# Kernel optimization log

Measured on AMD Instinct MI355X. Metric: run time of the kernel, lower is better.

## Reference

```python
import jax, jax.numpy as jnp
import numpy as np

# DH-SFNN: 2 dendritic LIF layers (denri, no tanh, reset-by-subtraction) + leaky readout integrator.
GAMMA = 0.5   # surrogate gradient scale
LENS = 0.5    # surrogate gradient width
VTH = 1.0     # spike threshold
DT = 1.0

@jax.custom_vjp
def spike_fn(x):
    # Heaviside forward, Gaussian surrogate backward (act_fun_adp)
    return (x > 0.0).astype(x.dtype)

def _spike_fwd(x):
    return spike_fn(x), x

def _spike_bwd(x, g):
    sg = GAMMA * jnp.exp(-x * x / (2.0 * LENS * LENS)) / (jnp.sqrt(2.0 * jnp.pi) * LENS)
    return (g * sg,)

spike_fn.defvjp(_spike_fwd, _spike_bwd)

B, T, IN, H, O, K = 256, 250, 700, 256, 20, 4  # batch, time, in_dim, hidden, out_dim, branch
WARMUP = 10


def _branch_mask(rng, out_dim, in_dim, k):
    # Each neuron's k branches see a disjoint random partition of the inputs.
    m = np.zeros((out_dim * k, in_dim), np.float32)
    step = in_dim // k
    for i in range(out_dim):
        perm = rng.permutation(in_dim)
        for j in range(k):
            m[i * k + j, perm[j * step:(j + 1) * step]] = 1.0
    return m


def setup_inputs() -> dict:
    key = jax.random.key(0)
    ks = jax.random.split(key, 12)
    rng = np.random.default_rng(0)
    s1 = 1.0 / np.sqrt(IN)
    s2 = 1.0 / np.sqrt(H)
    # branch-masked dense weights (apply_mask() already baked in)
    W1 = jax.random.uniform(ks[0], (H * K, IN), minval=-s1, maxval=s1) * jnp.asarray(_branch_mask(rng, H, IN, K))
    b1 = jax.random.uniform(ks[1], (H * K,), minval=-s1, maxval=s1)
    tau_n1 = jax.random.uniform(ks[2], (H, K), minval=2.0, maxval=6.0)
    tau_m1 = jax.random.uniform(ks[3], (H,), minval=0.0, maxval=4.0)
    W2 = jax.random.uniform(ks[4], (H * K, H), minval=-s2, maxval=s2) * jnp.asarray(_branch_mask(rng, H, H, K))
    b2 = jax.random.uniform(ks[5], (H * K,), minval=-s2, maxval=s2)
    tau_n2 = jax.random.uniform(ks[6], (H, K), minval=2.0, maxval=6.0)
    tau_m2 = jax.random.uniform(ks[7], (H,), minval=0.0, maxval=4.0)
    Wr = jax.random.uniform(ks[8], (O, H), minval=-s2, maxval=s2)
    br = jax.random.uniform(ks[9], (O,), minval=-s2, maxval=s2)
    tau_mr = jax.random.uniform(ks[10], (O,), minval=0.0, maxval=4.0)
    # sparse binary spike train input (SHD-like)
    x = (jax.random.uniform(ks[11], (B, T, IN)) < 0.1).astype(jnp.float32)
    return dict(x=x, W1=W1, b1=b1, tau_n1=tau_n1, tau_m1=tau_m1,
                W2=W2, b2=b2, tau_n2=tau_n2, tau_m2=tau_m2,
                Wr=Wr, br=br, tau_mr=tau_mr, warmup=WARMUP)


def reference(x, W1, b1, tau_n1, tau_m1, W2, b2, tau_n2, tau_m2, Wr, br, tau_mr, warmup):
    Bb, Tt, _ = x.shape
    beta1 = jax.nn.sigmoid(tau_n1)   # [H,K] dendritic decay
    alpha1 = jax.nn.sigmoid(tau_m1)  # [H]   soma decay
    beta2 = jax.nn.sigmoid(tau_n2)
    alpha2 = jax.nn.sigmoid(tau_m2)
    alphar = jax.nn.sigmoid(tau_mr)  # [O]

    def dense_branch(inp, W, b):
        return (inp @ W.T + b).reshape(inp.shape[0], -1, K)  # [B,H,K]

    def step(carry, xt):
        d1, m1, s1, d2, m2, s2, mr, acc, t = carry
        # layer 1: dendritic filtering then LIF with soft reset
        d1 = beta1 * d1 + (1.0 - beta1) * dense_branch(xt, W1, b1)
        m1 = m1 * alpha1 + (1.0 - alpha1) * DT * d1.sum(-1) - VTH * s1
        s1 = spike_fn(m1 - VTH)
        # layer 2
        d2 = beta2 * d2 + (1.0 - beta2) * dense_branch(s1, W2, b2)
        m2 = m2 * alpha2 + (1.0 - alpha2) * DT * d2.sum(-1) - VTH * s2
        s2 = spike_fn(m2 - VTH)
        # leaky readout integrator
        mr = mr * alphar + (1.0 - alphar) * (s2 @ Wr.T + br)
        acc = acc + jnp.where(t >= warmup, mr, jnp.zeros_like(mr))
        return (d1, m1, s1, d2, m2, s2, mr, acc, t + 1), None

    z = lambda *s: jnp.zeros(s, x.dtype)
    carry0 = (z(Bb, H, K), z(Bb, H), z(Bb, H),
              z(Bb, H, K), z(Bb, H), z(Bb, H),
              z(Bb, O), z(Bb, O), jnp.int32(0))
    carry, _ = jax.lax.scan(step, carry0, jnp.moveaxis(x, 1, 0))
    acc = carry[7]
    return acc / (Tt - warmup)  # readout_mode == 'mean'
```

## Files before the change

### kernel.cpp

```cpp
#include <hip/hip_runtime.h>
#include <hip/hip_bf16.h>

typedef unsigned short us16;
typedef unsigned int u32;
typedef unsigned long long ull;

#define B_   256
#define T_   250
#define IN_  700
#define KP_  704
#define H_   256
#define O_   20
#define HK_  1024
#define NPAIR_ (B_ * T_)
#define LDP_ 40
#define CP_  136

typedef __attribute__((ext_vector_type(8))) short short8;
typedef __attribute__((ext_vector_type(4))) float f32x4;

__device__ __forceinline__ float bfbits(unsigned int lo16) {
    union { unsigned int i; float f; } v; v.i = lo16 << 16; return v.f;
}
__device__ __forceinline__ float bflo(unsigned int u) {
    union { unsigned int i; float f; } v; v.i = u << 16; return v.f;
}
__device__ __forceinline__ float bfhi(unsigned int u) {
    union { unsigned int i; float f; } v; v.i = u & 0xffff0000u; return v.f;
}
__device__ __forceinline__ us16 f2bfu(float f) {
    __hip_bfloat16 h = __float2bfloat16(f);
    union { __hip_bfloat16 h; us16 u; } c; c.h = h; return c.u;
}
__device__ __forceinline__ float sigm(float x) { return 1.0f / (1.0f + expf(-x)); }
__device__ __forceinline__ int rfl(int v) { return __builtin_amdgcn_readfirstlane(v); }

__device__ __forceinline__ bool detect_bf16(const us16* __restrict__ taun) {
    int ok = 0;
#pragma unroll
    for (int i = 0; i < 8; i += 2) ok += ((taun[i] >> 8) == 0x40) ? 1 : 0;
    return ok == 4;
}
__device__ __forceinline__ float ldany(const void* __restrict__ p, long i, bool isb) {
    return isb ? bfbits(((const us16*)p)[i]) : ((const float*)p)[i];
}

__device__ __forceinline__ void async_cp16(const us16* g, us16* l) {
    __builtin_amdgcn_global_load_lds(
        (const __attribute__((address_space(1))) u32*)g,
        (__attribute__((address_space(3))) u32*)l, 16, 0, 0);
}

#define BAR_LDS() do {                                                   \
    asm volatile("s_waitcnt lgkmcnt(0)\n\ts_barrier" ::: "memory");      \
} while (0)

__global__ __launch_bounds__(256) void cvt_rows2(
    const void* __restrict__ xin, const void* __restrict__ w1in,
    us16* __restrict__ xout, us16* __restrict__ w1out,
    const us16* __restrict__ taun) {
    const bool isb = detect_bf16(taun);
    const int r = blockIdx.x * 4 + (threadIdx.x >> 6);
    const int l = threadIdx.x & 63;
    const void* in; us16* out; long ibase, obase;
    if (r < NPAIR_) {
        in = xin;  out = xout;  ibase = (long)r * IN_; obase = (long)r * KP_;
    } else {
        const int r2 = r - NPAIR_;
        if (r2 >= HK_) return;
        in = w1in; out = w1out; ibase = (long)r2 * IN_; obase = (long)r2 * KP_;
    }
    for (int c = l; c < 88; c += 64) {
        uint4 o;
        if (c < 87) {
            if (isb) {
                uint2 lo = *(const uint2*)((const us16*)in + ibase + 8 * c);
                uint2 hi = *(const uint2*)((const us16*)in + ibase + 8 * c + 4);
                o.x = lo.x; o.y = lo.y; o.z = hi.x; o.w = hi.y;
            } else {
                float4 f0 = *(const float4*)((const float*)in + ibase + 8 * c);
                float4 f1 = *(const float4*)((const float*)in + ibase + 8 * c + 4);
                o.x = (u32)f2bfu(f0.x) | ((u32)f2bfu(f0.y) << 16);
                o.y = (u32)f2bfu(f0.z) | ((u32)f2bfu(f0.w) << 16);
                o.z = (u32)f2bfu(f1.x) | ((u32)f2bfu(f1.y) << 16);
                o.w = (u32)f2bfu(f1.z) | ((u32)f2bfu(f1.w) << 16);
            }
        } else {
            o.z = 0u; o.w = 0u;
            if (isb) {
                uint2 lo = *(const uint2*)((const us16*)in + ibase + 696);
                o.x = lo.x; o.y = lo.y;
            } else {
                float4 f0 = *(const float4*)((const float*)in + ibase + 696);
                o.x = (u32)f2bfu(f0.x) | ((u32)f2bfu(f0.y) << 16);
                o.y = (u32)f2bfu(f0.z) | ((u32)f2bfu(f0.w) << 16);
            }
        }
        *(uint4*)(out + obase + 8 * c) = o;
    }
}

__global__ void transpose_to_bf16(const void* __restrict__ in, us16* __restrict__ out,
                                  int R, int C, const us16* __restrict__ taun) {
    const bool isb = detect_bf16(taun);
    __shared__ us16 tile[32][33];
    int c0 = blockIdx.x * 32, r0 = blockIdx.y * 32;
    int tx = threadIdx.x, ty = threadIdx.y;
#pragma unroll
// ... 65 lines not shown
    __syncthreads();

    for (int s = 0; s < 11; ++s) {
        const int cur = (s & 1) * 16384;
        const int nxt = 16384 - cur;
        if (s + 1 < 11) {
            const int kb = (s + 1) * 64;
#pragma unroll
            for (int i = 0; i < 4; ++i) async_cp16(xg[i] + kb, smem + nxt + asl[i]);
#pragma unroll
            for (int i = 0; i < 4; ++i) async_cp16(wg[i] + kb, smem + nxt + bsl[i]);
        }

        short8 af[4][2], bfv[4][2];
#pragma unroll
        for (int i = 0; i < 4; ++i) {
            af[i][0]  = *(const short8*)(smem + cur + aoff0[i]);
            af[i][1]  = *(const short8*)(smem + cur + aoff1[i]);
            bfv[i][0] = *(const short8*)(smem + cur + boff0[i]);
            bfv[i][1] = *(const short8*)(smem + cur + boff1[i]);
        }
#pragma unroll
        for (int h = 0; h < 2; ++h)
#pragma unroll
            for (int i = 0; i < 4; ++i)
#pragma unroll
                for (int j = 0; j < 4; ++j)
                    acc[i][j] = __builtin_amdgcn_mfma_f32_16x16x32_bf16(
                        af[i][h], bfv[j][h], acc[i][j], 0, 0, 0);

        __syncthreads();
    }

#pragma unroll
    for (int i = 0; i < 4; ++i)
#pragma unroll
        for (int j = 0; j < 4; ++j)
#pragma unroll
            for (int r = 0; r < 4; ++r)
                smem[(wr * 64 + i * 16 + quad * 4 + r) * CP_ +
                     (wc * 64 + j * 16 + l16)] = f2bfu(acc[i][j][r]);
    __syncthreads();
    {
        const int c8 = (lane & 15) * 8;
#pragma unroll
        for (int r2 = 0; r2 < 8; ++r2) {
            const int row = w * 32 + r2 * 4 + (lane >> 4);
            const uint4 v = *(const uint4*)(smem + row * CP_ + c8);
            *(uint4*)(Apre + (long)(m0 + row) * HK_ + n0 + c8) = v;
        }
    }
}

__global__ __launch_bounds__(256) void dhsfnn_4w(
    const us16* __restrict__ Apre,
    const void* __restrict__ b1,  const void* __restrict__ tau_n1,
    const void* __restrict__ tau_m1,
    const void* __restrict__ b2,  const void* __restrict__ tau_n2,
    const void* __restrict__ tau_m2,
    const void* __restrict__ Wr,  const void* __restrict__ br,
    const void* __restrict__ tau_mr,
    const us16* __restrict__ W2T,
    const int* __restrict__ warmup_p,
    void* __restrict__ out)
{
    __shared__ ull msk1[2][4];
    __shared__ ull msk2[2][4];

    const int tid  = threadIdx.x;
    const int lane = tid & 63;
    const int w    = tid >> 6;
    const int b    = blockIdx.x;
    const bool isb = detect_bf16((const us16*)tau_n1);
    const int wu   = *warmup_p;

    float be1[4], cb1[4], ce1[4], be2[4], cb2[4], ce2[4], d1[4], d2[4];
#pragma unroll
    for (int k = 0; k < 4; ++k) {
        const long gi = 4L * tid + k;
        const float t1 = sigm(ldany(tau_n1, gi, isb));
        be1[k] = t1; ce1[k] = 1.f - t1; cb1[k] = ce1[k] * ldany(b1, gi, isb);
        const float t2 = sigm(ldany(tau_n2, gi, isb));
        be2[k] = t2; ce2[k] = 1.f - t2; cb2[k] = ce2[k] * ldany(b2, gi, isb);
        d1[k] = 0.f; d2[k] = 0.f;
    }
    const float al1 = sigm(ldany(tau_m1, tid, isb)), cal1 = 1.f - al1;
    const float al2 = sigm(ldany(tau_m2, tid, isb)), cal2 = 1.f - al2;
    float m1 = 0.f, s1f = 0.f, m2 = 0.f, s2f = 0.f;
    float alr = 0.f, brv = 0.f;
    if (tid < O_) { alr = sigm(ldany(tau_mr, tid, isb)); brv = ldany(br, tid, isb); }
    float mrv = 0.f, accO = 0.f;

    const us16* ap = Apre + (long)b * T_ * HK_ + 4 * tid;

    uint2 q0 = *(const uint2*)(ap);
    uint2 q1 = *(const uint2*)(ap + HK_);
    uint2 q2 = *(const uint2*)(ap + 2 * HK_);
    uint2 q3 = *(const uint2*)(ap + 3 * HK_);

    {
        const float a0 = bflo(q0.x), a1 = bfhi(q0.x), a2 = bflo(q0.y), a3 = bfhi(q0.y);
        d1[0] = be1[0] * d1[0] + cb1[0] + ce1[0] * a0;
        d1[1] = be1[1] * d1[1] + cb1[1] + ce1[1] * a1;
        d1[2] = be1[2] * d1[2] + cb1[2] + ce1[2] * a2;
        d1[3] = be1[3] * d1[3] + cb1[3] + ce1[3] * a3;
        const float s = (d1[0] + d1[1]) + (d1[2] + d1[3]);
        m1 = m1 * al1 + cal1 * s - s1f;
        s1f = (m1 > 1.0f) ? 1.f : 0.f;
        const ull bm = __ballot(s1f > 0.f);
        if (lane == 0) msk1[0][w] = bm;
    }
    BAR_LDS();

    auto body = [&](int t, uint2& q, bool doL1) {
        const ull p0 = msk1[t & 1][0], p1 = msk1[t & 1][1];
        const ull p2 = msk1[t & 1][2], p3 = msk1[t & 1][3];
        d2[0] = be2[0] * d2[0] + cb2[0];
        d2[1] = be2[1] * d2[1] + cb2[1];
        d2[2] = be2[2] * d2[2] + cb2[2];
        d2[3] = be2[3] * d2[3] + cb2[3];
        if ((p0 | p1 | p2 | p3) != 0ull) {
            float g0 = 0.f, g1 = 0.f, g2 = 0.f, g3 = 0.f;
#pragma unroll
            for (int w2 = 0; w2 < 4; ++w2) {
                ull mm = (w2 == 0) ? p0 : (w2 == 1) ? p1 : (w2 == 2) ? p2 : p3;
                while (mm) {
                    const int i = __ffsll(mm) - 1; mm &= mm - 1;
                    const int n = 64 * w2 + i;
                    const uint2 wv = *(const uint2*)(W2T + ((long)n << 10) + 4 * tid);
                    g0 += bflo(wv.x); g1 += bfhi(wv.x);
                    g2 += bflo(wv.y); g3 += bfhi(wv.y);
                }
            }
            d2[0] += ce2[0] * g0; d2[1] += ce2[1] * g1;
            d2[2] += ce2[2] * g2; d2[3] += ce2[3] * g3;
        }
        const float s2s = (d2[0] + d2[1]) + (d2[2] + d2[3]);
        m2 = m2 * al2 + cal2 * s2s - s2f;
        s2f = (m2 > 1.0f) ? 1.f : 0.f;
        const ull b2m = __ballot(s2f > 0.f);
        if (lane == 0) msk2[t & 1][w] = b2m;

        if (doL1) {
            const float a0 = bflo(q.x), a1 = bfhi(q.x), a2 = bflo(q.y), a3 = bfhi(q.y);
            if (t + 5 < T_) q = *(const uint2*)(ap + (long)(t + 5) * HK_);
            d1[0] = be1[0] * d1[0] + cb1[0] + ce1[0] * a0;
            d1[1] = be1[1] * d1[1] + cb1[1] + ce1[1] * a1;
            d1[2] = be1[2] * d1[2] + cb1[2] + ce1[2] * a2;
            d1[3] = be1[3] * d1[3] + cb1[3] + ce1[3] * a3;
            const float s = (d1[0] + d1[1]) + (d1[2] + d1[3]);
            m1 = m1 * al1 + cal1 * s - s1f;
            s1f = (m1 > 1.0f) ? 1.f : 0.f;
            const ull b1m = __ballot(s1f > 0.f);
            if (lane == 0) msk1[(t + 1) & 1][w] = b1m;
        }

        BAR_LDS();

        if (w == 0) {
            const ull r0 = msk2[t & 1][0], r1 = msk2[t & 1][1];
            const ull r2 = msk2[t & 1][2], r3 = msk2[t & 1][3];
            if (lane < O_) {
                float sum = brv;
                if ((r0 | r1 | r2 | r3) != 0ull) {
#pragma unroll
                    for (int w2 = 0; w2 < 4; ++w2) {
                        ull mm = (w2 == 0) ? r0 : (w2 == 1) ? r1 : (w2 == 2) ? r2 : r3;
                        while (mm) {
                            const int i = __ffsll(mm) - 1; mm &= mm - 1;
                            sum += ldany(Wr, (long)lane * H_ + 64 * w2 + i, isb);
                        }
                    }
                }
                mrv = alr * mrv + (1.f - alr) * sum;
                if (t >= wu) accO += mrv;
            }
        }
    };

    int t = 0;
    for (int it = 0; it < 62; ++it) {
        body(t + 0, q1, true);
        body(t + 1, q2, true);
        body(t + 2, q3, true);
        body(t + 3, q0, true);
        t += 4;
    }
    body(248, q1, true);
    body(249, q2, false);

    if (tid < O_) {
        const float res = accO / (float)(T_ - wu);
        if (isb) ((us16*)out)[b * O_ + tid] = f2bfu(res);
        else     ((float*)out)[b * O_ + tid] = res;
    }
}

#define GA_LOAD(S, AV, BV) do {                                               \
    const int k0_ = (S) * 32 + half16;                                        \
    if (k0_ + 16 <= IN_) {                                                    \
        if (isb) {                                                            \
            const us16* pa_ = (const us16*)X  + arow + k0_;                   \
            const us16* pb_ = (const us16*)W1 + brow + k0_;                   \
            uint2 a0_ = *(const uint2*)pa_,        a1_ = *(const uint2*)(pa_ + 4);  \
            uint2 a2_ = *(const uint2*)(pa_ + 8),  a3_ = *(const uint2*)(pa_ + 12); \
            uint2 b0_ = *(const uint2*)pb_,        b1_ = *(const uint2*)(pb_ + 4);  \
            uint2 b2_ = *(const uint2*)(pb_ + 8),  b3_ = *(const uint2*)(pb_ + 12); \
            AV[0]=a0_.x; AV[1]=a0_.y; AV[2]=a1_.x; AV[3]=a1_.y;               \
            AV[4]=a2_.x; AV[5]=a2_.y; AV[6]=a3_.x; AV[7]=a3_.y;               \
            BV[0]=b0_.x; BV[1]=b0_.y; BV[2]=b1_.x; BV[3]=b1_.y;               \
            BV[4]=b2_.x; BV[5]=b2_.y; BV[6]=b3_.x; BV[7]=b3_.y;               \
        } else {                                                              \
            const float* pa_ = (const float*)X  + arow + k0_;                 \
            const float* pb_ = (const float*)W1 + brow + k0_;                 \
            float4 fa0_ = *(const float4*)pa_,        fa1_ = *(const float4*)(pa_ + 4);  \
            float4 fa2_ = *(const float4*)(pa_ + 8),  fa3_ = *(const float4*)(pa_ + 12); \
            float4 fb0_ = *(const float4*)pb_,        fb1_ = *(const float4*)(pb_ + 4);  \
            float4 fb2_ = *(const float4*)(pb_ + 8),  fb3_ = *(const float4*)(pb_ + 12); \
            AV[0] = (unsigned)f2bfu(fa0_.x) | ((unsigned)f2bfu(fa0_.y) << 16); \
            AV[1] = (unsigned)f2bfu(fa0_.z) | ((unsigned)f2bfu(fa0_.w) << 16); \
            AV[2] = (unsigned)f2bfu(fa1_.x) | ((unsigned)f2bfu(fa1_.y) << 16); \
            AV[3] = (unsigned)f2bfu(fa1_.z) | ((unsigned)f2bfu(fa1_.w) << 16); \
            AV[4] = (unsigned)f2bfu(fa2_.x) | ((unsigned)f2bfu(fa2_.y) << 16); \
            AV[5] = (unsigned)f2bfu(fa2_.z) | ((unsigned)f2bfu(fa2_.w) << 16); \
            AV[6] = (unsigned)f2bfu(fa3_.x) | ((unsigned)f2bfu(fa3_.y) << 16); \
            AV[7] = (unsigned)f2bfu(fa3_.z) | ((unsigned)f2bfu(fa3_.w) << 16); \
            BV[0] = (unsigned)f2bfu(fb0_.x) | ((unsigned)f2bfu(fb0_.y) << 16); \
            BV[1] = (unsigned)f2bfu(fb0_.z) | ((unsigned)f2bfu(fb0_.w) << 16); \
            BV[2] = (unsigned)f2bfu(fb1_.x) | ((unsigned)f2bfu(fb1_.y) << 16); \
            BV[3] = (unsigned)f2bfu(fb1_.z) | ((unsigned)f2bfu(fb1_.w) << 16); \
            BV[4] = (unsigned)f2bfu(fb2_.x) | ((unsigned)f2bfu(fb2_.y) << 16); \
            BV[5] = (unsigned)f2bfu(fb2_.z) | ((unsigned)f2bfu(fb2_.w) << 16); \
            BV[6] = (unsigned)f2bfu(fb3_.x) | ((unsigned)f2bfu(fb3_.y) << 16); \
            BV[7] = (unsigned)f2bfu(fb3_.z) | ((unsigned)f2bfu(fb3_.w) << 16); \
        }                                                                     \
    } else {                                                                  \
        _Pragma("unroll")                                                     \
        for (int e_ = 0; e_ < 8; ++e_) { AV[e_] = 0u; BV[e_] = 0u; }          \
        _Pragma("unroll")                                                     \
        for (int e_ = 0; e_ < 16; ++e_) {                                     \
            int k_ = k0_ + e_;                                                \
            if (k_ < IN_) {                                                   \
                unsigned va_ = (unsigned)f2bfu(ldany(X,  arow + k_, isb));    \
                unsigned vb_ = (unsigned)f2bfu(ldany(W1, brow + k_, isb));    \
                AV[e_ >> 1] |= va_ << ((e_ & 1) * 16);                        \
                BV[e_ >> 1] |= vb_ << ((e_ & 1) * 16);                        \
            }                                                                 \
// ... 60 lines not shown
    }

    const long arow = (long)(m0 + ra) * IN_;
    const long brow = (long)(n0 + ra) * IN_;
    us16* asw = As + ra * LDP_ + half16;
    us16* bsw = Bs + ra * LDP_ + half16;

    unsigned av0[8], bv0[8], av1[8], bv1[8];
    GA_LOAD(0, av0, bv0);

    for (int ss = 0; ss < 11; ++ss) {
        __syncthreads();
        GA_STORE(av0, bv0);
        __syncthreads();
        GA_LOAD(2 * ss + 1, av1, bv1);
        GA_MFMA();
        __syncthreads();
        GA_STORE(av1, bv1);
        __syncthreads();
        if (ss < 10) GA_LOAD(2 * ss + 2, av0, bv0);
        GA_MFMA();
    }

#pragma unroll
    for (int i = 0; i < 4; ++i) {
#pragma unroll
        for (int j = 0; j < 4; ++j) {
            const int gm = m0 + wr * 64 + i * 16 + quad * 4;
            const int gn = n0 + wc * 64 + j * 16 + l16;
            us16* op = Apre + (long)gm * HK_ + gn;
#pragma unroll
            for (int r = 0; r < 4; ++r)
                op[(long)r * HK_] = f2bfu(acc[i][j][r]);
        }
    }
}

__global__ __launch_bounds__(64) void dhsfnn_wave(
    const us16* __restrict__ Apre,
    const void* __restrict__ b1,  const void* __restrict__ tau_n1,
    const void* __restrict__ tau_m1,
    const void* __restrict__ b2,  const void* __restrict__ tau_n2,
    const void* __restrict__ tau_m2,
    const void* __restrict__ Wr,  const void* __restrict__ br,
    const void* __restrict__ tau_mr,
    const us16* __restrict__ W2T,
    const int* __restrict__ warmup_p,
    void* __restrict__ out)
{
    const int lane = threadIdx.x;
    const int b    = blockIdx.x;
    const bool isb = detect_bf16((const us16*)tau_n1);
    const int wu   = *warmup_p;

    float be1[16], cb1[16], be2[16], cb2[16], d1[16], d2[16];
#pragma unroll
    for (int e = 0; e < 16; ++e) {
        const long gi = (long)lane * 16 + e;
        const float t1 = sigm(ldany(tau_n1, gi, isb));
        be1[e] = t1; cb1[e] = (1.f - t1) * ldany(b1, gi, isb);
        const float t2 = sigm(ldany(tau_n2, gi, isb));
        be2[e] = t2; cb2[e] = (1.f - t2) * ldany(b2, gi, isb);
        d1[e] = 0.f; d2[e] = 0.f;
    }
    float al1[4], al2[4], m1[4], s1[4], m2[4], s2[4];
#pragma unroll
    for (int j = 0; j < 4; ++j) {
        al1[j] = sigm(ldany(tau_m1, lane * 4 + j, isb));
        al2[j] = sigm(ldany(tau_m2, lane * 4 + j, isb));
        m1[j] = 0.f; s1[j] = 0.f; m2[j] = 0.f; s2[j] = 0.f;
    }
    float alr = 0.f, brv = 0.f;
    if (lane < O_) { alr = sigm(ldany(tau_mr, lane, isb)); brv = ldany(br, lane, isb); }
    float mrv = 0.f, accO = 0.f;

    const us16* ap = Apre + (long)b * T_ * HK_ + lane * 16;

    auto wstep = [&](int t, uint4 lo, uint4 hi) {
        float a[16];
        a[0]=bflo(lo.x);  a[1]=bfhi(lo.x);  a[2]=bflo(lo.y);  a[3]=bfhi(lo.y);
        a[4]=bflo(lo.z);  a[5]=bfhi(lo.z);  a[6]=bflo(lo.w);  a[7]=bfhi(lo.w);
        a[8]=bflo(hi.x);  a[9]=bfhi(hi.x);  a[10]=bflo(hi.y); a[11]=bfhi(hi.y);
        a[12]=bflo(hi.z); a[13]=bfhi(hi.z); a[14]=bflo(hi.w); a[15]=bfhi(hi.w);
#pragma unroll
        for (int e = 0; e < 16; ++e)
            d1[e] = be1[e] * d1[e] + cb1[e] + (1.f - be1[e]) * a[e];
        unsigned long long bal1[4];
#pragma unroll
        for (int j = 0; j < 4; ++j) {
            const float s = (d1[j*4+0] + d1[j*4+1]) + (d1[j*4+2] + d1[j*4+3]);
            m1[j] = m1[j] * al1[j] + (1.f - al1[j]) * s - s1[j];
            s1[j] = (m1[j] > 1.0f) ? 1.f : 0.f;
            bal1[j] = __ballot(s1[j] > 0.f);
        }
        if ((bal1[0] | bal1[1] | bal1[2] | bal1[3]) != 0ull) {
            float g[16];
#pragma unroll
            for (int e = 0; e < 16; ++e) g[e] = 0.f;
            for (int j2 = 0; j2 < 4; ++j2) {
                unsigned long long mm = bal1[j2];
                while (mm) {
                    const int i = __ffsll(mm) - 1; mm &= mm - 1;
                    const us16* wv = W2T + ((long)(i * 4 + j2) << 10) + lane * 16;
                    const uint4 wl = *(const uint4*)wv;
                    const uint4 wh = *(const uint4*)(wv + 8);
                    g[0]+=bflo(wl.x);  g[1]+=bfhi(wl.x);  g[2]+=bflo(wl.y);  g[3]+=bfhi(wl.y);
                    g[4]+=bflo(wl.z);  g[5]+=bfhi(wl.z);  g[6]+=bflo(wl.w);  g[7]+=bfhi(wl.w);
                    g[8]+=bflo(wh.x);  g[9]+=bfhi(wh.x);  g[10]+=bflo(wh.y); g[11]+=bfhi(wh.y);
                    g[12]+=bflo(wh.z); g[13]+=bfhi(wh.z); g[14]+=bflo(wh.w); g[15]+=bfhi(wh.w);
                }
            }
#pragma unroll
            for (int e = 0; e < 16; ++e)
                d2[e] = be2[e] * d2[e] + cb2[e] + (1.f - be2[e]) * g[e];
        } else {
#pragma unroll
            for (int e = 0; e < 16; ++e)
                d2[e] = be2[e] * d2[e] + cb2[e];
        }
        unsigned long long bal2[4];
#pragma unroll
        for (int j = 0; j < 4; ++j) {
            const float s = (d2[j*4+0] + d2[j*4+1]) + (d2[j*4+2] + d2[j*4+3]);
            m2[j] = m2[j] * al2[j] + (1.f - al2[j]) * s - s2[j];
            s2[j] = (m2[j] > 1.0f) ? 1.f : 0.f;
            bal2[j] = __ballot(s2[j] > 0.f);
        }
        if (lane < O_) {
            float sum = brv;
            if ((bal2[0] | bal2[1] | bal2[2] | bal2[3]) != 0ull) {
                for (int j2 = 0; j2 < 4; ++j2) {
                    unsigned long long mm = bal2[j2];
                    while (mm) {
                        const int i = __ffsll(mm) - 1; mm &= mm - 1;
                        sum += ldany(Wr, (long)lane * H_ + (i * 4 + j2), isb);
                    }
                }
            }
            mrv = alr * mrv + (1.f - alr) * sum;
            if (t >= wu) accO += mrv;
        }
    };

    uint4 q0a = *(const uint4*)(ap);
    uint4 q0b = *(const uint4*)(ap + 8);
    uint4 q1a = *(const uint4*)(ap + HK_);
    uint4 q1b = *(const uint4*)(ap + HK_ + 8);
    uint4 q2a = *(const uint4*)(ap + 2 * HK_);
    uint4 q2b = *(const uint4*)(ap + 2 * HK_ + 8);
    uint4 q3a = *(const uint4*)(ap + 3 * HK_);
    uint4 q3b = *(const uint4*)(ap + 3 * HK_ + 8);

    int t = 0;
    for (int it = 0; it < 62; ++it) {
        wstep(t + 0, q0a, q0b);
        q0a = *(const uint4*)(ap + (long)(t + 4) * HK_);
        q0b = *(const uint4*)(ap + (long)(t + 4) * HK_ + 8);
        wstep(t + 1, q1a, q1b);
        if (t + 5 < T_) {
            q1a = *(const uint4*)(ap + (long)(t + 5) * HK_);
            q1b = *(const uint4*)(ap + (long)(t + 5) * HK_ + 8);
        }
        wstep(t + 2, q2a, q2b);
        if (t + 6 < T_) {
            q2a = *(const uint4*)(ap + (long)(t + 6) * HK_);
            q2b = *(const uint4*)(ap + (long)(t + 6) * HK_ + 8);
        }
        wstep(t + 3, q3a, q3b);
        if (t + 7 < T_) {
            q3a = *(const uint4*)(ap + (long)(t + 7) * HK_);
            q3b = *(const uint4*)(ap + (long)(t + 7) * HK_ + 8);
        }
        t += 4;
    }
    wstep(248, q0a, q0b);
    wstep(249, q1a, q1b);

    if (lane < O_) {
        const float res = accO / (float)(T_ - wu);
        if (isb) ((us16*)out)[b * O_ + lane] = f2bfu(res);
        else     ((float*)out)[b * O_ + lane] = res;
    }
}

__global__ __launch_bounds__(256) void dhsfnn_fb(
    const void* __restrict__ x,  const void* __restrict__ W1,
    const void* __restrict__ b1, const void* __restrict__ tau_n1,
    const void* __restrict__ tau_m1,
    const void* __restrict__ W2, const void* __restrict__ b2,
    const void* __restrict__ tau_n2, const void* __restrict__ tau_m2,
    const void* __restrict__ Wr, const void* __restrict__ br,
    const void* __restrict__ tau_mr,
    const int* __restrict__ warmup_p,
    void* __restrict__ out)
{
    __shared__ us16 list1[1024];
    __shared__ us16 list2[256];
    __shared__ us16 list3[256];
    __shared__ int n1s, n2s, n3s;

    const int tid = threadIdx.x;
    const int b   = blockIdx.x;
    const int h   = tid;
    const bool isb = detect_bf16((const us16*)tau_n1);
    const int wu  = *warmup_p;

    const float be1_0 = sigm(ldany(tau_n1, 4 * h + 0, isb));
    const float be1_1 = sigm(ldany(tau_n1, 4 * h + 1, isb));
    const float be1_2 = sigm(ldany(tau_n1, 4 * h + 2, isb));
    const float be1_3 = sigm(ldany(tau_n1, 4 * h + 3, isb));
    const float bi1_0 = ldany(b1, 4 * h + 0, isb), bi1_1 = ldany(b1, 4 * h + 1, isb);
    const float bi1_2 = ldany(b1, 4 * h + 2, isb), bi1_3 = ldany(b1, 4 * h + 3, isb);
    const float al1 = sigm(ldany(tau_m1, h, isb));
    const float be2_0 = sigm(ldany(tau_n2, 4 * h + 0, isb));
    const float be2_1 = sigm(ldany(tau_n2, 4 * h + 1, isb));
    const float be2_2 = sigm(ldany(tau_n2, 4 * h + 2, isb));
    const float be2_3 = sigm(ldany(tau_n2, 4 * h + 3, isb));
    const float bi2_0 = ldany(b2, 4 * h + 0, isb), bi2_1 = ldany(b2, 4 * h + 1, isb);
    const float bi2_2 = ldany(b2, 4 * h + 2, isb), bi2_3 = ldany(b2, 4 * h + 3, isb);
    const float al2 = sigm(ldany(tau_m2, h, isb));
    float alr = 0.f, brv = 0.f;
    if (h < O_) { alr = sigm(ldany(tau_mr, h, isb)); brv = ldany(br, h, isb); }

    float d1_0 = 0.f, d1_1 = 0.f, d1_2 = 0.f, d1_3 = 0.f, m1v = 0.f, s1f = 0.f;
    float d2_0 = 0.f, d2_1 = 0.f, d2_2 = 0.f, d2_3 = 0.f, m2v = 0.f, s2f = 0.f;
    float mrv = 0.f, accO = 0.f;

    const long xbase = (long)b * T_ * IN_;
    float xv0 = ldany(x, xbase + tid, isb);
    float xv1 = ldany(x, xbase + tid + 256, isb);
    float xv2 = (tid + 512 < IN_) ? ldany(x, xbase + tid + 512, isb) : 0.f;

    for (int t = 0; t < T_; ++t) {
        const bool p0 = xv0 != 0.f, p1 = xv1 != 0.f, p2 = xv2 != 0.f;
        if (t + 1 < T_) {
// ... 55 lines not shown
        __syncthreads();
        int n3 = n3s; n3 = (n3 < 256) ? n3 : 256;

        if (h < O_) {
            float sum = brv;
            for (int idx = 0; idx < n3; ++idx) {
                int j = (int)list3[idx];
                j = (j < H_) ? j : (H_ - 1);
                sum += ldany(Wr, (long)h * H_ + j, isb);
            }
            mrv = alr * mrv + (1.f - alr) * sum;
            if (t >= wu) accO += mrv;
        }
    }
    if (h < O_) {
        float res = accO / (float)(T_ - wu);
        if (isb) ((us16*)out)[b * O_ + h] = f2bfu(res);
        else     ((float*)out)[b * O_ + h] = res;
    }
}

extern "C" void kernel_launch(void* const* d_in, const int* in_sizes, int n_in,
                              void* d_out, int out_size, void* d_ws, size_t ws_size,
                              hipStream_t stream) {
    const void* x      = d_in[0];
    const void* W1     = d_in[1];
    const void* b1     = d_in[2];
    const void* tau_n1 = d_in[3];
    const void* tau_m1 = d_in[4];
    const void* W2     = d_in[5];
    const void* b2     = d_in[6];
    const void* tau_n2 = d_in[7];
    const void* tau_m2 = d_in[8];
    const void* Wr     = d_in[9];
    const void* br     = d_in[10];
    const void* tau_mr = d_in[11];
    const int*  warmup = (const int*)d_in[12];

    const size_t w2t_bytes  = (size_t)H_ * HK_ * 2;
    const size_t xbf_bytes  = (size_t)NPAIR_ * KP_ * 2;
    const size_t w1b_bytes  = (size_t)HK_ * KP_ * 2;
    const size_t apre_bytes = (size_t)NPAIR_ * HK_ * 2;

    const bool tier0 = (d_ws != nullptr &&
                        ws_size >= w2t_bytes + xbf_bytes + w1b_bytes + apre_bytes);
    const bool tier1 = (d_ws != nullptr && ws_size >= w2t_bytes + apre_bytes);

    dim3 blk(32, 8);
    if (tier0) {
        us16* W2T  = (us16*)d_ws;
        us16* Xbf  = (us16*)((char*)d_ws + w2t_bytes);
        us16* W1bf = (us16*)((char*)d_ws + w2t_bytes + xbf_bytes);
        us16* Apre = (us16*)((char*)d_ws + w2t_bytes + xbf_bytes + w1b_bytes);
        cvt_rows2<<<(NPAIR_ + HK_) / 4, 256, 0, stream>>>(
            x, W1, Xbf, W1bf, (const us16*)tau_n1);
        transpose_to_bf16<<<dim3((H_ + 31) / 32, (HK_ + 31) / 32), blk, 0, stream>>>(
            W2, W2T, HK_, H_, (const us16*)tau_n1);
        gemm_bf<<<4096, 256, 0, stream>>>(Xbf, W1bf, Apre);
        dhsfnn_4w<<<B_, 256, 0, stream>>>(
            Apre, b1, tau_n1, tau_m1, b2, tau_n2, tau_m2,
            Wr, br, tau_mr, W2T, warmup, d_out);
    } else if (tier1) {
        us16* W2T  = (us16*)d_ws;
        us16* Apre = (us16*)((char*)d_ws + w2t_bytes);
        transpose_to_bf16<<<dim3((H_ + 31) / 32, (HK_ + 31) / 32), blk, 0, stream>>>(
            W2, W2T, HK_, H_, (const us16*)tau_n1);
        gemm_apre<<<4096, 256, 0, stream>>>(x, W1, (const us16*)tau_n1, Apre);
        dhsfnn_wave<<<B_, 64, 0, stream>>>(
            Apre, b1, tau_n1, tau_m1, b2, tau_n2, tau_m2,
            Wr, br, tau_mr, W2T, warmup, d_out);
    } else {
        dhsfnn_fb<<<B_, 256, 0, stream>>>(x, W1, b1, tau_n1, tau_m1,
                                          W2, b2, tau_n2, tau_m2,
                                          Wr, br, tau_mr, warmup, d_out);
    }
}
```

Measured before the change: 456.1 us.

## Split recurrence into layer-1 spike check and conditional full recurrence

Measured after the change: 409.6 us. -10.2%, faster.

```diff
diff --git a/kernel.cpp b/kernel.cpp
--- a/kernel.cpp
+++ b/kernel.cpp
@@ -50,10 +50,6 @@
         (const __attribute__((address_space(1))) u32*)g,
         (__attribute__((address_space(3))) u32*)l, 16, 0, 0);
 }
-
-#define BAR_LDS() do {                                                   \
-    asm volatile("s_waitcnt lgkmcnt(0)\n\ts_barrier" ::: "memory");      \
-} while (0)
 
 __global__ __launch_bounds__(256) void cvt_rows2(
     const void* __restrict__ xin, const void* __restrict__ w1in,
@@ -225,7 +221,272 @@
     }
 }
 
-__global__ __launch_bounds__(256) void dhsfnn_4w(
+__device__ void wave_recur(
+    const us16* __restrict__ Apre,
+    const void* __restrict__ b1,  const void* __restrict__ tau_n1,
+    const void* __restrict__ tau_m1,
+    const void* __restrict__ b2,  const void* __restrict__ tau_n2,
+    const void* __restrict__ tau_m2,
+    const void* __restrict__ Wr,  const void* __restrict__ br,
+    const void* __restrict__ tau_mr,
+    const us16* __restrict__ W2T,
+    int wu, bool isb, int b, int lane,
+    void* __restrict__ out)
+{
+    float be1[16], cb1[16], be2[16], cb2[16], d1[16], d2[16];
+#pragma unroll
+    for (int e = 0; e < 16; ++e) {
+        const long gi = (long)lane * 16 + e;
+        const float t1 = sigm(ldany(tau_n1, gi, isb));
+        be1[e] = t1; cb1[e] = (1.f - t1) * ldany(b1, gi, isb);
+        const float t2 = sigm(ldany(tau_n2, gi, isb));
+        be2[e] = t2; cb2[e] = (1.f - t2) * ldany(b2, gi, isb);
+        d1[e] = 0.f; d2[e] = 0.f;
+    }
+    float al1[4], al2[4], m1[4], s1[4], m2[4], s2[4];
+#pragma unroll
+    for (int j = 0; j < 4; ++j) {
+        al1[j] = sigm(ldany(tau_m1, lane * 4 + j, isb));
+        al2[j] = sigm(ldany(tau_m2, lane * 4 + j, isb));
+        m1[j] = 0.f; s1[j] = 0.f; m2[j] = 0.f; s2[j] = 0.f;
+    }
+    float alr = 0.f, brv = 0.f;
+    if (lane < O_) { alr = sigm(ldany(tau_mr, lane, isb)); brv = ldany(br, lane, isb); }
+    float mrv = 0.f, accO = 0.f;
+
+    const us16* ap = Apre + (long)b * T_ * HK_ + lane * 16;
+
+    auto wstep = [&](int t, uint4 lo, uint4 hi) {
+        float a[16];
+        a[0]=bflo(lo.x);  a[1]=bfhi(lo.x);  a[2]=bflo(lo.y);  a[3]=bfhi(lo.y);
+        a[4]=bflo(lo.z);  a[5]=bfhi(lo.z);  a[6]=bflo(lo.w);  a[7]=bfhi(lo.w);
+        a[8]=bflo(hi.x);  a[9]=bfhi(hi.x);  a[10]=bflo(hi.y); a[11]=bfhi(hi.y);
+        a[12]=bflo(hi.z); a[13]=bfhi(hi.z); a[14]=bflo(hi.w); a[15]=bfhi(hi.w);
+#pragma unroll
+        for (int e = 0; e < 16; ++e)
+            d1[e] = be1[e] * d1[e] + cb1[e] + (1.f - be1[e]) * a[e];
+        unsigned long long bal1[4];
+#pragma unroll
+        for (int j = 0; j < 4; ++j) {
+            const float s = (d1[j*4+0] + d1[j*4+1]) + (d1[j*4+2] + d1[j*4+3]);
+            m1[j] = m1[j] * al1[j] + (1.f - al1[j]) * s - s1[j];
+            s1[j] = (m1[j] > 1.0f) ? 1.f : 0.f;
+            bal1[j] = __ballot(s1[j] > 0.f);
+        }
+        if ((bal1[0] | bal1[1] | bal1[2] | bal1[3]) != 0ull) {
+            float g[16];
+#pragma unroll
+            for (int e = 0; e < 16; ++e) g[e] = 0.f;
+            for (int j2 = 0; j2 < 4; ++j2) {
+                unsigned long long mm = bal1[j2];
+                while (mm) {
+                    const int i = __ffsll(mm) - 1; mm &= mm - 1;
+                    const us16* wv = W2T + ((long)(i * 4 + j2) << 10) + lane * 16;
+                    const uint4 wl = *(const uint4*)wv;
+                    const uint4 wh = *(const uint4*)(wv + 8);
+                    g[0]+=bflo(wl.x);  g[1]+=bfhi(wl.x);  g[2]+=bflo(wl.y);  g[3]+=bfhi(wl.y);
+                    g[4]+=bflo(wl.z);  g[5]+=bfhi(wl.z);  g[6]+=bflo(wl.w);  g[7]+=bfhi(wl.w);
+                    g[8]+=bflo(wh.x);  g[9]+=bfhi(wh.x);  g[10]+=bflo(wh.y); g[11]+=bfhi(wh.y);
+                    g[12]+=bflo(wh.z); g[13]+=bfhi(wh.z); g[14]+=bflo(wh.w); g[15]+=bfhi(wh.w);
+                }
+            }
+#pragma unroll
+            for (int e = 0; e < 16; ++e)
+                d2[e] = be2[e] * d2[e] + cb2[e] + (1.f - be2[e]) * g[e];
+        } else {
+#pragma unroll
+            for (int e = 0; e < 16; ++e)
+                d2[e] = be2[e] * d2[e] + cb2[e];
+        }
+        unsigned long long bal2[4];
+#pragma unroll
+        for (int j = 0; j < 4; ++j) {
+            const float s = (d2[j*4+0] + d2[j*4+1]) + (d2[j*4+2] + d2[j*4+3]);
+            m2[j] = m2[j] * al2[j] + (1.f - al2[j]) * s - s2[j];
+            s2[j] = (m2[j] > 1.0f) ? 1.f : 0.f;
+            bal2[j] = __ballot(s2[j] > 0.f);
+        }
+        if (lane < O_) {
+            float sum = brv;
+            if ((bal2[0] | bal2[1] | bal2[2] | bal2[3]) != 0ull) {
+                for (int j2 = 0; j2 < 4; ++j2) {
+                    unsigned long long mm = bal2[j2];
+                    while (mm) {
+                        const int i = __ffsll(mm) - 1; mm &= mm - 1;
+                        sum += ldany(Wr, (long)lane * H_ + (i * 4 + j2), isb);
+                    }
+                }
+            }
+            mrv = alr * mrv + (1.f - alr) * sum;
+            if (t >= wu) accO += mrv;
+        }
+    };
+
+    uint4 q0a = *(const uint4*)(ap);
+    uint4 q0b = *(const uint4*)(ap + 8);
+    uint4 q1a = *(const uint4*)(ap + HK_);
+    uint4 q1b = *(const uint4*)(ap + HK_ + 8);
+    uint4 q2a = *(const uint4*)(ap + 2 * HK_);
+    uint4 q2b = *(const uint4*)(ap + 2 * HK_ + 8);
+    uint4 q3a = *(const uint4*)(ap + 3 * HK_);
+    uint4 q3b = *(const uint4*)(ap + 3 * HK_ + 8);
+
+    int t = 0;
+    for (int it = 0; it < 62; ++it) {
+        wstep(t + 0, q0a, q0b);
+        q0a = *(const uint4*)(ap + (long)(t + 4) * HK_);
+        q0b = *(const uint4*)(ap + (long)(t + 4) * HK_ + 8);
+        wstep(t + 1, q1a, q1b);
+        if (t + 5 < T_) {
+            q1a = *(const uint4*)(ap + (long)(t + 5) * HK_);
+            q1b = *(const uint4*)(ap + (long)(t + 5) * HK_ + 8);
+        }
+        wstep(t + 2, q2a, q2b);
+        if (t + 6 < T_) {
+            q2a = *(const uint4*)(ap + (long)(t + 6) * HK_);
+            q2b = *(const uint4*)(ap + (long)(t + 6) * HK_ + 8);
+        }
+        wstep(t + 3, q3a, q3b);
+        if (t + 7 < T_) {
+            q3a = *(const uint4*)(ap + (long)(t + 7) * HK_);
+            q3b = *(const uint4*)(ap + (long)(t + 7) * HK_ + 8);
+        }
+        t += 4;
+    }
+    wstep(248, q0a, q0b);
+    wstep(249, q1a, q1b);
+
+    if (lane < O_) {
+        const float res = accO / (float)(T_ - wu);
+        if (isb) ((us16*)out)[b * O_ + lane] = f2bfu(res);
+        else     ((float*)out)[b * O_ + lane] = res;
+    }
+}
+
+__global__ __launch_bounds__(256) void l1_check(
+    const us16* __restrict__ Apre,
+    const void* __restrict__ b1,  const void* __restrict__ tau_n1,
+    const void* __restrict__ tau_m1,
+    const void* __restrict__ b2,  const void* __restrict__ tau_n2,
+    const void* __restrict__ tau_m2,
+    const void* __restrict__ Wr,  const void* __restrict__ br,
+    const void* __restrict__ tau_mr,
+    const int* __restrict__ warmup_p,
+    int* __restrict__ flags, float* __restrict__ sh_out)
+{
+    const int tid = threadIdx.x;
+    const int b   = blockIdx.x;
+    const bool isb = detect_bf16((const us16*)tau_n1);
+
+    if (b == B_) {
+        if (tid >= 64) return;
+        const int lane = tid;
+        const int wu   = *warmup_p;
+        float be2[16], cb2[16], d2[16];
+#pragma unroll
+        for (int e = 0; e < 16; ++e) {
+            const long gi = (long)lane * 16 + e;
+            const float t2 = sigm(ldany(tau_n2, gi, isb));
+            be2[e] = t2; cb2[e] = (1.f - t2) * ldany(b2, gi, isb);
+            d2[e] = 0.f;
+        }
+        float al2[4], m2[4], s2[4];
+#pragma unroll
+        for (int j = 0; j < 4; ++j) {
+            al2[j] = sigm(ldany(tau_m2, lane * 4 + j, isb));
+            m2[j] = 0.f; s2[j] = 0.f;
+        }
+        float alr = 0.f, brv = 0.f;
+        if (lane < O_) { alr = sigm(ldany(tau_mr, lane, isb)); brv = ldany(br, lane, isb); }
+        float mrv = 0.f, accO = 0.f;
+
+        for (int t = 0; t < T_; ++t) {
+#pragma unroll
+            for (int e = 0; e < 16; ++e)
+                d2[e] = be2[e] * d2[e] + cb2[e];
+            unsigned long long bal2[4];
+#pragma unroll
+            for (int j = 0; j < 4; ++j) {
+                const float s = (d2[j*4+0] + d2[j*4+1]) + (d2[j*4+2] + d2[j*4+3]);
+                m2[j] = m2[j] * al2[j] + (1.f - al2[j]) * s - s2[j];
+                s2[j] = (m2[j] > 1.0f) ? 1.f : 0.f;
+                bal2[j] = __ballot(s2[j] > 0.f);
+            }
+            if (lane < O_) {
+                float sum = brv;
+                if ((bal2[0] | bal2[1] | bal2[2] | bal2[3]) != 0ull) {
+                    for (int j2 = 0; j2 < 4; ++j2) {
+                        unsigned long long mm = bal2[j2];
+                        while (mm) {
+                            const int i = __ffsll(mm) - 1; mm &= mm - 1;
+                            sum += ldany(Wr, (long)lane * H_ + (i * 4 + j2), isb);
+                        }
+                    }
+                }
+                mrv = alr * mrv + (1.f - alr) * sum;
+                if (t >= wu) accO += mrv;
+            }
+        }
+        if (lane < O_) sh_out[lane] = accO / (float)(T_ - wu);
+        return;
+    }
+
+    __shared__ int blkflag;
+    if (tid == 0) blkflag = 0;
+    __syncthreads();
+
+    float be1[4], cb1[4], ce1[4], d1[4];
+#pragma unroll
+    for (int k = 0; k < 4; ++k) {
+        const long gi = 4L * tid + k;
+        const float t1 = sigm(ldany(tau_n1, gi, isb));
+        be1[k] = t1; ce1[k] = 1.f - t1; cb1[k] = ce1[k] * ldany(b1, gi, isb);
+        d1[k] = 0.f;
+    }
+    const float al1 = sigm(ldany(tau_m1, tid, isb)), cal1 = 1.f - al1;
+    float m1 = 0.f, s1f = 0.f;
+    int any = 0;
+
+    const us16* ap = Apre + (long)b * T_ * HK_ + 4 * tid;
+
+    uint2 q0 = *(const uint2*)(ap);
+    uint2 q1 = *(const uint2*)(ap + HK_);
+    uint2 q2 = *(const uint2*)(ap + 2 * HK_);
+    uint2 q3 = *(const uint2*)(ap + 3 * HK_);
+    uint2 q4 = *(const uint2*)(ap + 4 * HK_);
+    uint2 q5 = *(const uint2*)(ap + 5 * HK_);
+    uint2 q6 = *(const uint2*)(ap + 6 * HK_);
+    uint2 q7 = *(const uint2*)(ap + 7 * HK_);
+
+    auto body = [&](int t, uint2& q) {
+        const float a0 = bflo(q.x), a1 = bfhi(q.x), a2 = bflo(q.y), a3 = bfhi(q.y);
+        if (t + 8 < T_) q = *(const uint2*)(ap + (long)(t + 8) * HK_);
+        d1[0] = be1[0] * d1[0] + cb1[0] + ce1[0] * a0;
+        d1[1] = be1[1] * d1[1] + cb1[1] + ce1[1] * a1;
+        d1[2] = be1[2] * d1[2] + cb1[2] + ce1[2] * a2;
+        d1[3] = be1[3] * d1[3] + cb1[3] + ce1[3] * a3;
+        const float s = (d1[0] + d1[1]) + (d1[2] + d1[3]);
+        m1 = m1 * al1 + cal1 * s - s1f;
+        const int sp = (m1 > 1.0f) ? 1 : 0;
+        s1f = sp ? 1.f : 0.f;
+        any |= sp;
+    };
+
+    int t = 0;
+    for (int it = 0; it < 31; ++it) {
+        body(t + 0, q0); body(t + 1, q1); body(t + 2, q2); body(t + 3, q3);
+        body(t + 4, q4); body(t + 5, q5); body(t + 6, q6); body(t + 7, q7);
+        t += 8;
+    }
+    body(248, q0);
+    body(249, q1);
+
+    if (any) blkflag = 1;
+    __syncthreads();
+    if (tid == 0) flags[b] = blkflag;
+}
+
+__global__ __launch_bounds__(64) void finalize(
     const us16* __restrict__ Apre,
     const void* __restrict__ b1,  const void* __restrict__ tau_n1,
     const void* __restrict__ tau_m1,
@@ -235,137 +496,21 @@
     const void* __restrict__ tau_mr,
     const us16* __restrict__ W2T,
     const int* __restrict__ warmup_p,
+    const int* __restrict__ flags, const float* __restrict__ sh_out,
     void* __restrict__ out)
 {
-    __shared__ ull msk1[2][4];
-    __shared__ ull msk2[2][4];
-
-    const int tid  = threadIdx.x;
-    const int lane = tid & 63;
-    const int w    = tid >> 6;
+    const int lane = threadIdx.x;
     const int b    = blockIdx.x;
     const bool isb = detect_bf16((const us16*)tau_n1);
     const int wu   = *warmup_p;
 
-    float be1[4], cb1[4], ce1[4], be2[4], cb2[4], ce2[4], d1[4], d2[4];
-#pragma unroll
-    for (int k = 0; k < 4; ++k) {
-        const long gi = 4L * tid + k;
-        const float t1 = sigm(ldany(tau_n1, gi, isb));
-        be1[k] = t1; ce1[k] = 1.f - t1; cb1[k] = ce1[k] * ldany(b1, gi, isb);
-        const float t2 = sigm(ldany(tau_n2, gi, isb));
-        be2[k] = t2; ce2[k] = 1.f - t2; cb2[k] = ce2[k] * ldany(b2, gi, isb);
-        d1[k] = 0.f; d2[k] = 0.f;
-    }
-    const float al1 = sigm(ldany(tau_m1, tid, isb)), cal1 = 1.f - al1;
-    const float al2 = sigm(ldany(tau_m2, tid, isb)), cal2 = 1.f - al2;
-    float m1 = 0.f, s1f = 0.f, m2 = 0.f, s2f = 0.f;
-    float alr = 0.f, brv = 0.f;
-    if (tid < O_) { alr = sigm(ldany(tau_mr, tid, isb)); brv = ldany(br, tid, isb); }
-    float mrv = 0.f, accO = 0.f;
-
-    const us16* ap = Apre + (long)b * T_ * HK_ + 4 * tid;
-
-    uint2 q0 = *(const uint2*)(ap);
-    uint2 q1 = *(const uint2*)(ap + HK_);
-    uint2 q2 = *(const uint2*)(ap + 2 * HK_);
-    uint2 q3 = *(const uint2*)(ap + 3 * HK_);
-
-    {
-        const float a0 = bflo(q0.x), a1 = bfhi(q0.x), a2 = bflo(q0.y), a3 = bfhi(q0.y);
-        d1[0] = be1[0] * d1[0] + cb1[0] + ce1[0] * a0;
-        d1[1] = be1[1] * d1[1] + cb1[1] + ce1[1] * a1;
-        d1[2] = be1[2] * d1[2] + cb1[2] + ce1[2] * a2;
-        d1[3] = be1[3] * d1[3] + cb1[3] + ce1[3] * a3;
-        const float s = (d1[0] + d1[1]) + (d1[2] + d1[3]);
-        m1 = m1 * al1 + cal1 * s - s1f;
-        s1f = (m1 > 1.0f) ? 1.f : 0.f;
-        const ull bm = __ballot(s1f > 0.f);
-        if (lane == 0) msk1[0][w] = bm;
-    }
-    BAR_LDS();
-
-    auto body = [&](int t, uint2& q, bool doL1) {
-        const ull p0 = msk1[t & 1][0], p1 = msk1[t & 1][1];
-        const ull p2 = msk1[t & 1][2], p3 = msk1[t & 1][3];
-        d2[0] = be2[0] * d2[0] + cb2[0];
-        d2[1] = be2[1] * d2[1] + cb2[1];
-        d2[2] = be2[2] * d2[2] + cb2[2];
-        d2[3] = be2[3] * d2[3] + cb2[3];
-        if ((p0 | p1 | p2 | p3) != 0ull) {
-            float g0 = 0.f, g1 = 0.f, g2 = 0.f, g3 = 0.f;
-#pragma unroll
-            for (int w2 = 0; w2 < 4; ++w2) {
-                ull mm = (w2 == 0) ? p0 : (w2 == 1) ? p1 : (w2 == 2) ? p2 : p3;
-                while (mm) {
-                    const int i = __ffsll(mm) - 1; mm &= mm - 1;
-                    const int n = 64 * w2 + i;
-                    const uint2 wv = *(const uint2*)(W2T + ((long)n << 10) + 4 * tid);
-                    g0 += bflo(wv.x); g1 += bfhi(wv.x);
-                    g2 += bflo(wv.y); g3 += bfhi(wv.y);
-                }
-            }
-            d2[0] += ce2[0] * g0; d2[1] += ce2[1] * g1;
-            d2[2] += ce2[2] * g2; d2[3] += ce2[3] * g3;
-        }
-        const float s2s = (d2[0] + d2[1]) + (d2[2] + d2[3]);
-        m2 = m2 * al2 + cal2 * s2s - s2f;
-        s2f = (m2 > 1.0f) ? 1.f : 0.f;
-        const ull b2m = __ballot(s2f > 0.f);
-        if (lane == 0) msk2[t & 1][w] = b2m;
-
-        if (doL1) {
-            const float a0 = bflo(q.x), a1 = bfhi(q.x), a2 = bflo(q.y), a3 = bfhi(q.y);
-            if (t + 5 < T_) q = *(const uint2*)(ap + (long)(t + 5) * HK_);
-            d1[0] = be1[0] * d1[0] + cb1[0] + ce1[0] * a0;
-            d1[1] = be1[1] * d1[1] + cb1[1] + ce1[1] * a1;
-            d1[2] = be1[2] * d1[2] + cb1[2] + ce1[2] * a2;
-            d1[3] = be1[3] * d1[3] + cb1[3] + ce1[3] * a3;
-            const float s = (d1[0] + d1[1]) + (d1[2] + d1[3]);
-            m1 = m1 * al1 + cal1 * s - s1f;
-            s1f = (m1 > 1.0f) ? 1.f : 0.f;
-            const ull b1m = __ballot(s1f > 0.f);
-            if (lane == 0) msk1[(t + 1) & 1][w] = b1m;
-        }
-
-        BAR_LDS();
-
-        if (w == 0) {
-            const ull r0 = msk2[t & 1][0], r1 = msk2[t & 1][1];
-            const ull r2 = msk2[t & 1][2], r3 = msk2[t & 1][3];
-            if (lane < O_) {
-                float sum = brv;
-                if ((r0 | r1 | r2 | r3) != 0ull) {
-#pragma unroll
-                    for (int w2 = 0; w2 < 4; ++w2) {
-                        ull mm = (w2 == 0) ? r0 : (w2 == 1) ? r1 : (w2 == 2) ? r2 : r3;
-                        while (mm) {
-                            const int i = __ffsll(mm) - 1; mm &= mm - 1;
-                            sum += ldany(Wr, (long)lane * H_ + 64 * w2 + i, isb);
-                        }
-                    }
-                }
-                mrv = alr * mrv + (1.f - alr) * sum;
-                if (t >= wu) accO += mrv;
-            }
-        }
-    };
-
-    int t = 0;
-    for (int it = 0; it < 62; ++it) {
-        body(t + 0, q1, true);
-        body(t + 1, q2, true);
-        body(t + 2, q3, true);
-        body(t + 3, q0, true);
-        t += 4;
-    }
-    body(248, q1, true);
-    body(249, q2, false);
-
-    if (tid < O_) {
-        const float res = accO / (float)(T_ - wu);
-        if (isb) ((us16*)out)[b * O_ + tid] = f2bfu(res);
-        else     ((float*)out)[b * O_ + tid] = res;
+    if (flags[b]) {
+        wave_recur(Apre, b1, tau_n1, tau_m1, b2, tau_n2, tau_m2,
+                   Wr, br, tau_mr, W2T, wu, isb, b, lane, out);
+    } else if (lane < O_) {
+        const float res = sh_out[lane];
+        if (isb) ((us16*)out)[b * O_ + lane] = f2bfu(res);
+        else     ((float*)out)[b * O_ + lane] = res;
     }
 }
 
@@ -532,135 +677,8 @@
     const int b    = blockIdx.x;
     const bool isb = detect_bf16((const us16*)tau_n1);
     const int wu   = *warmup_p;
-
-    float be1[16], cb1[16], be2[16], cb2[16], d1[16], d2[16];
-#pragma unroll
-    for (int e = 0; e < 16; ++e) {
-        const long gi = (long)lane * 16 + e;
-        const float t1 = sigm(ldany(tau_n1, gi, isb));
-        be1[e] = t1; cb1[e] = (1.f - t1) * ldany(b1, gi, isb);
-        const float t2 = sigm(ldany(tau_n2, gi, isb));
-        be2[e] = t2; cb2[e] = (1.f - t2) * ldany(b2, gi, isb);
-        d1[e] = 0.f; d2[e] = 0.f;
-    }
-    float al1[4], al2[4], m1[4], s1[4], m2[4], s2[4];
-#pragma unroll
-    for (int j = 0; j < 4; ++j) {
-        al1[j] = sigm(ldany(tau_m1, lane * 4 + j, isb));
-        al2[j] = sigm(ldany(tau_m2, lane * 4 + j, isb));
-        m1[j] = 0.f; s1[j] = 0.f; m2[j] = 0.f; s2[j] = 0.f;
-    }
-    float alr = 0.f, brv = 0.f;
-    if (lane < O_) { alr = sigm(ldany(tau_mr, lane, isb)); brv = ldany(br, lane, isb); }
-    float mrv = 0.f, accO = 0.f;
-
-    const us16* ap = Apre + (long)b * T_ * HK_ + lane * 16;
-
-    auto wstep = [&](int t, uint4 lo, uint4 hi) {
-        float a[16];
-        a[0]=bflo(lo.x);  a[1]=bfhi(lo.x);  a[2]=bflo(lo.y);  a[3]=bfhi(lo.y);
-        a[4]=bflo(lo.z);  a[5]=bfhi(lo.z);  a[6]=bflo(lo.w);  a[7]=bfhi(lo.w);
-        a[8]=bflo(hi.x);  a[9]=bfhi(hi.x);  a[10]=bflo(hi.y); a[11]=bfhi(hi.y);
-        a[12]=bflo(hi.z); a[13]=bfhi(hi.z); a[14]=bflo(hi.w); a[15]=bfhi(hi.w);
-#pragma unroll
-        for (int e = 0; e < 16; ++e)
-            d1[e] = be1[e] * d1[e] + cb1[e] + (1.f - be1[e]) * a[e];
-        unsigned long long bal1[4];
-#pragma unroll
-        for (int j = 0; j < 4; ++j) {
-            const float s = (d1[j*4+0] + d1[j*4+1]) + (d1[j*4+2] + d1[j*4+3]);
-            m1[j] = m1[j] * al1[j] + (1.f - al1[j]) * s - s1[j];
-            s1[j] = (m1[j] > 1.0f) ? 1.f : 0.f;
-            bal1[j] = __ballot(s1[j] > 0.f);
-        }
-        if ((bal1[0] | bal1[1] | bal1[2] | bal1[3]) != 0ull) {
-            float g[16];
-#pragma unroll
-            for (int e = 0; e < 16; ++e) g[e] = 0.f;
-            for (int j2 = 0; j2 < 4; ++j2) {
-                unsigned long long mm = bal1[j2];
-                while (mm) {
-                    const int i = __ffsll(mm) - 1; mm &= mm - 1;
-                    const us16* wv = W2T + ((long)(i * 4 + j2) << 10) + lane * 16;
-                    const uint4 wl = *(const uint4*)wv;
-                    const uint4 wh = *(const uint4*)(wv + 8);
-                    g[0]+=bflo(wl.x);  g[1]+=bfhi(wl.x);  g[2]+=bflo(wl.y);  g[3]+=bfhi(wl.y);
-                    g[4]+=bflo(wl.z);  g[5]+=bfhi(wl.z);  g[6]+=bflo(wl.w);  g[7]+=bfhi(wl.w);
-                    g[8]+=bflo(wh.x);  g[9]+=bfhi(wh.x);  g[10]+=bflo(wh.y); g[11]+=bfhi(wh.y);
-                    g[12]+=bflo(wh.z); g[13]+=bfhi(wh.z); g[14]+=bflo(wh.w); g[15]+=bfhi(wh.w);
-                }
-            }
-#pragma unroll
-            for (int e = 0; e < 16; ++e)
-                d2[e] = be2[e] * d2[e] + cb2[e] + (1.f - be2[e]) * g[e];
-        } else {
-#pragma unroll
-            for (int e = 0; e < 16; ++e)
-                d2[e] = be2[e] * d2[e] + cb2[e];
-        }
-        unsigned long long bal2[4];
-#pragma unroll
-        for (int j = 0; j < 4; ++j) {
-            const float s = (d2[j*4+0] + d2[j*4+1]) + (d2[j*4+2] + d2[j*4+3]);
-            m2[j] = m2[j] * al2[j] + (1.f - al2[j]) * s - s2[j];
-            s2[j] = (m2[j] > 1.0f) ? 1.f : 0.f;
-            bal2[j] = __ballot(s2[j] > 0.f);
-        }
-        if (lane < O_) {
-            float sum = brv;
-            if ((bal2[0] | bal2[1] | bal2[2] | bal2[3]) != 0ull) {
-                for (int j2 = 0; j2 < 4; ++j2) {
-                    unsigned long long mm = bal2[j2];
-                    while (mm) {
-                        const int i = __ffsll(mm) - 1; mm &= mm - 1;
-                        sum += ldany(Wr, (long)lane * H_ + (i * 4 + j2), isb);
-                    }
-                }
-            }
-            mrv = alr * mrv + (1.f - alr) * sum;
-            if (t >= wu) accO += mrv;
-        }
-    };
-
-    uint4 q0a = *(const uint4*)(ap);
-    uint4 q0b = *(const uint4*)(ap + 8);
-    uint4 q1a = *(const uint4*)(ap + HK_);
-    uint4 q1b = *(const uint4*)(ap + HK_ + 8);
-    uint4 q2a = *(const uint4*)(ap + 2 * HK_);
-    uint4 q2b = *(const uint4*)(ap + 2 * HK_ + 8);
-    uint4 q3a = *(const uint4*)(ap + 3 * HK_);
-    uint4 q3b = *(const uint4*)(ap + 3 * HK_ + 8);
-
-    int t = 0;
-    for (int it = 0; it < 62; ++it) {
-        wstep(t + 0, q0a, q0b);
-        q0a = *(const uint4*)(ap + (long)(t + 4) * HK_);
-        q0b = *(const uint4*)(ap + (long)(t + 4) * HK_ + 8);
-        wstep(t + 1, q1a, q1b);
-        if (t + 5 < T_) {
-            q1a = *(const uint4*)(ap + (long)(t + 5) * HK_);
-            q1b = *(const uint4*)(ap + (long)(t + 5) * HK_ + 8);
-        }
-        wstep(t + 2, q2a, q2b);
-        if (t + 6 < T_) {
-            q2a = *(const uint4*)(ap + (long)(t + 6) * HK_);
-            q2b = *(const uint4*)(ap + (long)(t + 6) * HK_ + 8);
-        }
-        wstep(t + 3, q3a, q3b);
-        if (t + 7 < T_) {
-            q3a = *(const uint4*)(ap + (long)(t + 7) * HK_);
-            q3b = *(const uint4*)(ap + (long)(t + 7) * HK_ + 8);
-        }
-        t += 4;
-    }
-    wstep(248, q0a, q0b);
-    wstep(249, q1a, q1b);
-
-    if (lane < O_) {
-        const float res = accO / (float)(T_ - wu);
-        if (isb) ((us16*)out)[b * O_ + lane] = f2bfu(res);
-        else     ((float*)out)[b * O_ + lane] = res;
-    }
+    wave_recur(Apre, b1, tau_n1, tau_m1, b2, tau_n2, tau_m2,
+               Wr, br, tau_mr, W2T, wu, isb, b, lane, out);
 }
 
 __global__ __launch_bounds__(256) void dhsfnn_fb(
@@ -822,14 +840,20 @@
         us16* Xbf  = (us16*)((char*)d_ws + w2t_bytes);
         us16* W1bf = (us16*)((char*)d_ws + w2t_bytes + xbf_bytes);
         us16* Apre = (us16*)((char*)d_ws + w2t_bytes + xbf_bytes + w1b_bytes);
+        int*   flags  = (int*)Xbf;
+        float* sh_out = (float*)(Xbf + 2048);
+
         cvt_rows2<<<(NPAIR_ + HK_) / 4, 256, 0, stream>>>(
             x, W1, Xbf, W1bf, (const us16*)tau_n1);
         transpose_to_bf16<<<dim3((H_ + 31) / 32, (HK_ + 31) / 32), blk, 0, stream>>>(
             W2, W2T, HK_, H_, (const us16*)tau_n1);
         gemm_bf<<<4096, 256, 0, stream>>>(Xbf, W1bf, Apre);
-        dhsfnn_4w<<<B_, 256, 0, stream>>>(
+        l1_check<<<B_ + 1, 256, 0, stream>>>(
             Apre, b1, tau_n1, tau_m1, b2, tau_n2, tau_m2,
-            Wr, br, tau_mr, W2T, warmup, d_out);
+            Wr, br, tau_mr, warmup, flags, sh_out);
+        finalize<<<B_, 64, 0, stream>>>(
+            Apre, b1, tau_n1, tau_m1, b2, tau_n2, tau_m2,
+            Wr, br, tau_mr, W2T, warmup, flags, sh_out, d_out);
     } else if (tier1) {
         us16* W2T  = (us16*)d_ws;
         us16* Apre = (us16*)((char*)d_ws + w2t_bytes);
```
